# Kernel tuning notes

Measured on AMD Instinct MI355X. Metric: run time of the kernel, lower is better.

The kernel has to match this reference:

```python
import jax, jax.numpy as jnp
import numpy as np

N = 100000      # nodes
E = 1600000     # edges (avg degree 16)
F_IN = 48       # input features
H = 64          # hidden
C = 2           # classes


def _init(key, shape, fan_in):
    return jax.random.normal(key, shape, jnp.float32) * (1.0 / np.sqrt(fan_in))


def setup_inputs() -> dict:
    key = jax.random.key(0)
    ks = jax.random.split(key, 12)
    return {
        "x": jax.random.normal(ks[0], (N, F_IN), jnp.float32),
        "edge_index": jax.random.randint(ks[1], (2, E), 0, N, dtype=jnp.int64),
        "W1l": _init(ks[2], (F_IN, H), F_IN),
        "b1l": jnp.zeros((H,), jnp.float32),
        "W1r": _init(ks[3], (F_IN, H), F_IN),
        "W2l": _init(ks[4], (H, H), H),
        "b2l": jnp.zeros((H,), jnp.float32),
        "W2r": _init(ks[5], (H, H), H),
        "Wlin1": _init(ks[6], (H, H), H),
        "blin1": jnp.zeros((H,), jnp.float32),
        "Wlin2": _init(ks[7], (H, C), H),
        "blin2": jnp.zeros((C,), jnp.float32),
    }


def _sage_conv(x, src, dst, Wl, bl, Wr, num_nodes):
    # mean aggregation of source-node features onto destination nodes
    msg = x[src]                                              # [E, F] gather
    agg = jax.ops.segment_sum(msg, dst, num_segments=num_nodes)
    cnt = jax.ops.segment_sum(jnp.ones((dst.shape[0], 1), x.dtype), dst,
                              num_segments=num_nodes)
    mean = agg / jnp.maximum(cnt, 1.0)
    # PyG SAGEConv: lin_l(aggr) + lin_r(root); bias only on lin_l
    return mean @ Wl + bl + x @ Wr


def reference(x, edge_index, W1l, b1l, W1r, W2l, b2l, W2r,
              Wlin1, blin1, Wlin2, blin2):
    src, dst = edge_index[0], edge_index[1]
    n = x.shape[0]
    h = jax.nn.sigmoid(_sage_conv(x, src, dst, W1l, b1l, W1r, n))
    h = jax.nn.sigmoid(_sage_conv(h, src, dst, W2l, b2l, W2r, n))
    # dropout(p=0.5) is identity in eval mode (self.training=False)
    h = jax.nn.sigmoid(h @ Wlin1 + blin1)
    return jax.nn.softmax(h @ Wlin2 + blin2, axis=1)
```

## Files before the change

kernel.cpp:

```cpp
#include <hip/hip_runtime.h>
#include <math.h>


#define NF1 48
#define HH 64
#define BKT_SHIFT 8
#define BKT_SZ (1 << BKT_SHIFT)
#define BCAP 4800
#define EPB 16

typedef __attribute__((ext_vector_type(8))) short short8v;
typedef __attribute__((ext_vector_type(4))) float float4v;

__device__ __forceinline__ float sigmoidf_(float v) {
  return 1.0f / (1.0f + __expf(-v));
}
__device__ __forceinline__ float bflo(unsigned w) {
  union { unsigned u; float f; } c; c.u = w << 16; return c.f;
}
__device__ __forceinline__ float bfhi(unsigned w) {
  union { unsigned u; float f; } c; c.u = w & 0xffff0000u; return c.f;
}
__device__ __forceinline__ unsigned short f2bf(float f) {
  union { float f; unsigned u; } c; c.f = f;
  unsigned r = c.u + 0x7fffu + ((c.u >> 16) & 1u);
  return (unsigned short)(r >> 16);
}

template <int K>
__global__ __launch_bounds__(256, 4) void fused_bin_gemm(
    const int* __restrict__ ei, int* __restrict__ cursor,
    unsigned* __restrict__ bins, int E, int NB,
    const float* __restrict__ X, const float* __restrict__ Wl,
    const float* __restrict__ Wr, const float* __restrict__ bias,
    unsigned short* __restrict__ t_out, float* __restrict__ r_out,
    int n_nodes, int abk, int gemmb) {
  __shared__ __align__(16) char smem[3 * 64 * 72 * 2];

  if ((int)blockIdx.x < abk) {
    int* hist = (int*)smem;
    int* gbase = hist + 512;
    for (int i = threadIdx.x; i < NB; i += 256) hist[i] = 0;
    __syncthreads();
    int base_e = blockIdx.x * (256 * EPB) + threadIdx.x;
    unsigned pk[EPB];
    int bk[EPB], rk[EPB];
#pragma unroll
    for (int k = 0; k < EPB; k++) {
      int e = base_e + k * 256;
      bk[k] = -1;
      if (e < E) {
        int s = ei[e], d = ei[E + e];
        int b = d >> BKT_SHIFT;
        pk[k] = ((unsigned)(d & (BKT_SZ - 1)) << 23) | (unsigned)s;
        bk[k] = b;
        rk[k] = atomicAdd(&hist[b], 1);
      }
    }
    __syncthreads();
    for (int i = threadIdx.x; i < NB; i += 256) {
      int c = hist[i];
      gbase[i] = (c > 0) ? atomicAdd(&cursor[i], c) : 0;
    }
    __syncthreads();
#pragma unroll
    for (int k = 0; k < EPB; k++) {
      if (bk[k] >= 0) {
        int pos = gbase[bk[k]] + rk[k];
        bins[(size_t)bk[k] * BCAP + pos] = pk[k];
      }
    }
    return;
  }

  short(*sA)[72] = (short(*)[72])smem;
  short(*sWl)[72] = (short(*)[72])(smem + 9216);
  short(*sWr)[72] = (short(*)[72])(smem + 18432);
  int gbid = (int)blockIdx.x - abk;
  int lane = threadIdx.x & 63, wv = threadIdx.x >> 6;
  int l15 = lane & 15, kq = lane >> 4;

  for (int i = threadIdx.x; i < 64 * 64; i += 256) {
    int k = i >> 6, j = i & 63;
    short vl = 0, vr = 0;
    if (k < K) {
      vl = (short)f2bf(Wl[k * 64 + j]);
      vr = (short)f2bf(Wr[k * 64 + j]);
    }
    sWl[j][k] = vl;
    sWr[j][k] = vr;
  }
  if (K < 64) {
    constexpr int PADW = (64 - K) / 2;
    for (int i = threadIdx.x; i < 64 * PADW; i += 256) {
      int row = i / PADW, p = i % PADW;
      *(unsigned*)&sA[row][K + 2 * p] = 0u;
    }
  }
  float bcol[4];
#pragma unroll
  for (int c = 0; c < 4; c++) bcol[c] = bias[c * 16 + l15];

  for (int nbase = gbid * 64; nbase < n_nodes; nbase += gemmb * 64) {
    __syncthreads();
    for (int i = threadIdx.x; i < 64 * (K / 4); i += 256) {
      int row = i / (K / 4), c4 = i % (K / 4);
      int rr = nbase + row;
      if (rr >= n_nodes) rr = n_nodes - 1;
      float4 xv = ((const float4*)(X + (size_t)rr * K))[c4];
      unsigned lo = ((unsigned)f2bf(xv.y) << 16) | (unsigned)f2bf(xv.x);
      unsigned hi = ((unsigned)f2bf(xv.w) << 16) | (unsigned)f2bf(xv.z);
      uint2 pk2 = {lo, hi};
      *(uint2*)&sA[row][c4 * 4] = pk2;
    }
    __syncthreads();

    float4v acc_t[4], acc_r[4];
#pragma unroll
    for (int c = 0; c < 4; c++) {
      acc_t[c] = (float4v){0.0f, 0.0f, 0.0f, 0.0f};
      acc_r[c] = (float4v){bcol[c], bcol[c], bcol[c], bcol[c]};
    }
#pragma unroll
    for (int s = 0; s < 2; s++) {
      short8v af = *(const short8v*)&sA[wv * 16 + l15][s * 32 + kq * 8];
#pragma unroll
      for (int c = 0; c < 4; c++) {
        short8v bl = *(const short8v*)&sWl[c * 16 + l15][s * 32 + kq * 8];
        short8v br = *(const short8v*)&sWr[c * 16 + l15][s * 32 + kq * 8];
        acc_t[c] = __builtin_amdgcn_mfma_f32_16x16x32_bf16(af, bl, acc_t[c], 0, 0, 0);
        acc_r[c] = __builtin_amdgcn_mfma_f32_16x16x32_bf16(af, br, acc_r[c], 0, 0, 0);
      }
    }
#pragma unroll
    for (int c = 0; c < 4; c++) {
      int j = c * 16 + l15;
#pragma unroll
      for (int g = 0; g < 4; g++) {
        int node = nbase + wv * 16 + kq * 4 + g;
        if (node < n_nodes) {
          t_out[(size_t)node * HH + j] = f2bf(acc_t[c][g]);
          r_out[(size_t)node * HH + j] = acc_r[c][g];
        }
      }
    }
  }
}

__global__ __launch_bounds__(256) void build_csr2(
    const unsigned* __restrict__ bins, const int* __restrict__ cursor,
    int* __restrict__ rp, int* __restrict__ csr, int n_nodes, int E, int NB) {
  __shared__ int hist[BKT_SZ];
  __shared__ int aa[BKT_SZ], bb[BKT_SZ];
  __shared__ int cur[BKT_SZ];
  int b = blockIdx.x;
  int tid = threadIdx.x;
  int node0 = b << BKT_SHIFT;
  int cnt = cursor[b];
  const unsigned* bp = bins + (size_t)b * BCAP;

  int part = 0;
  for (int i = tid; i < b; i += 256) part += cursor[i];
  aa[tid] = part;
  __syncthreads();
  for (int off = 128; off > 0; off >>= 1) {
    if (tid < off) aa[tid] += aa[tid + off];
    __syncthreads();
  }
  int gb = aa[0];
  __syncthreads();

  hist[tid] = 0;
  __syncthreads();
  for (int i = tid; i < cnt; i += 256) {
    atomicAdd(&hist[bp[i] >> 23], 1);
  }
  __syncthreads();
  int v = hist[tid];
  aa[tid] = v;
  __syncthreads();
  int* s = aa;
  int* d = bb;
  for (int off = 1; off < BKT_SZ; off <<= 1) {
    int t = s[tid] + ((tid >= off) ? s[tid - off] : 0);
    d[tid] = t;
    __syncthreads();
    int* tmp = s; s = d; d = tmp;
  }
  int loc = s[tid] - v;
  int node = node0 + tid;
  if (node < n_nodes) rp[node] = gb + loc;
  if (b == NB - 1 && tid == 0) rp[n_nodes] = E;
  cur[tid] = gb + loc;
  __syncthreads();
  for (int i = tid; i < cnt; i += 256) {
    unsigned p = bp[i];
    int dl = (int)(p >> 23);
    int pos = atomicAdd(&cur[dl], 1);
    csr[pos] = (int)(p & 0x7FFFFFu);
  }
}

__device__ __forceinline__ void gather8(const uint4* __restrict__ tb,
                                        const int* __restrict__ csr,
                                        int rs, int re, float* __restrict__ a) {
  int j = rs;
  for (; j + 7 < re; j += 8) {
    uint4 u0 = tb[(size_t)csr[j + 0] * 8];
    uint4 u1 = tb[(size_t)csr[j + 1] * 8];
    uint4 u2 = tb[(size_t)csr[j + 2] * 8];
    uint4 u3 = tb[(size_t)csr[j + 3] * 8];
    uint4 u4 = tb[(size_t)csr[j + 4] * 8];
    uint4 u5 = tb[(size_t)csr[j + 5] * 8];
    uint4 u6 = tb[(size_t)csr[j + 6] * 8];
    uint4 u7 = tb[(size_t)csr[j + 7] * 8];
    a[0] += ((bflo(u0.x) + bflo(u1.x)) + (bflo(u2.x) + bflo(u3.x))) +
            ((bflo(u4.x) + bflo(u5.x)) + (bflo(u6.x) + bflo(u7.x)));
    a[1] += ((bfhi(u0.x) + bfhi(u1.x)) + (bfhi(u2.x) + bfhi(u3.x))) +
            ((bfhi(u4.x) + bfhi(u5.x)) + (bfhi(u6.x) + bfhi(u7.x)));
    a[2] += ((bflo(u0.y) + bflo(u1.y)) + (bflo(u2.y) + bflo(u3.y))) +
            ((bflo(u4.y) + bflo(u5.y)) + (bflo(u6.y) + bflo(u7.y)));
    a[3] += ((bfhi(u0.y) + bfhi(u1.y)) + (bfhi(u2.y) + bfhi(u3.y))) +
            ((bfhi(u4.y) + bfhi(u5.y)) + (bfhi(u6.y) + bfhi(u7.y)));
    a[4] += ((bflo(u0.z) + bflo(u1.z)) + (bflo(u2.z) + bflo(u3.z))) +
            ((bflo(u4.z) + bflo(u5.z)) + (bflo(u6.z) + bflo(u7.z)));
    a[5] += ((bfhi(u0.z) + bfhi(u1.z)) + (bfhi(u2.z) + bfhi(u3.z))) +
            ((bfhi(u4.z) + bfhi(u5.z)) + (bfhi(u6.z) + bfhi(u7.z)));
    a[6] += ((bflo(u0.w) + bflo(u1.w)) + (bflo(u2.w) + bflo(u3.w))) +
            ((bflo(u4.w) + bflo(u5.w)) + (bflo(u6.w) + bflo(u7.w)));
    a[7] += ((bfhi(u0.w) + bfhi(u1.w)) + (bfhi(u2.w) + bfhi(u3.w))) +
            ((bfhi(u4.w) + bfhi(u5.w)) + (bfhi(u6.w) + bfhi(u7.w)));
  }
  if (j + 3 < re) {
    uint4 u0 = tb[(size_t)csr[j + 0] * 8];
    uint4 u1 = tb[(size_t)csr[j + 1] * 8];
    uint4 u2 = tb[(size_t)csr[j + 2] * 8];
    uint4 u3 = tb[(size_t)csr[j + 3] * 8];
    a[0] += (bflo(u0.x) + bflo(u1.x)) + (bflo(u2.x) + bflo(u3.x));
    a[1] += (bfhi(u0.x) + bfhi(u1.x)) + (bfhi(u2.x) + bfhi(u3.x));
    a[2] += (bflo(u0.y) + bflo(u1.y)) + (bflo(u2.y) + bflo(u3.y));
    a[3] += (bfhi(u0.y) + bfhi(u1.y)) + (bfhi(u2.y) + bfhi(u3.y));
    a[4] += (bflo(u0.z) + bflo(u1.z)) + (bflo(u2.z) + bflo(u3.z));
    a[5] += (bfhi(u0.z) + bfhi(u1.z)) + (bfhi(u2.z) + bfhi(u3.z));
    a[6] += (bflo(u0.w) + bflo(u1.w)) + (bflo(u2.w) + bflo(u3.w));
    a[7] += (bfhi(u0.w) + bfhi(u1.w)) + (bfhi(u2.w) + bfhi(u3.w));
    j += 4;
  }
  for (; j < re; j++) {
    uint4 u = tb[(size_t)csr[j] * 8];
    a[0] += bflo(u.x);
    a[1] += bfhi(u.x);
    a[2] += bflo(u.y);
    a[3] += bfhi(u.y);
    a[4] += bflo(u.z);
    a[5] += bfhi(u.z);
    a[6] += bflo(u.w);
    a[7] += bfhi(u.w);
  }
}

__global__ __launch_bounds__(256, 4) void fused_agg_gemm(
    const unsigned short* __restrict__ t1, const float* __restrict__ r1,
    const int* __restrict__ rp, const int* __restrict__ csr,
    const float* __restrict__ W2l, const float* __restrict__ W2r,
    const float* __restrict__ b2l,
    unsigned short* __restrict__ t2, unsigned short* __restrict__ r2,
    int n_nodes, int gemmb) {
  __shared__ short sA[64][72];
  __shared__ short sWl[64][72];
  __shared__ short sWr[64][72];
  int lane = threadIdx.x & 63, wv = threadIdx.x >> 6;
  int l15 = lane & 15, kq = lane >> 4;
  int grp8 = threadIdx.x >> 3, q8 = threadIdx.x & 7;

  for (int i = threadIdx.x; i < 64 * 64; i += 256) {
    int k = i >> 6, j = i & 63;
    sWl[j][k] = (short)f2bf(W2l[k * 64 + j]);
    sWr[j][k] = (short)f2bf(W2r[k * 64 + j]);
  }
  float bcol[4];
#pragma unroll
  for (int c = 0; c < 4; c++) bcol[c] = b2l[c * 16 + l15];

  for (int nbase = blockIdx.x * 64; nbase < n_nodes; nbase += gemmb * 64) {
    __syncthreads();
#pragma unroll
    for (int p = 0; p < 2; p++) {
      int row = p * 32 + grp8;
      int node = nbase + row;
      int nn = node < n_nodes ? node : n_nodes - 1;
      int rs = rp[nn], re = rp[nn + 1];
      int deg = re - rs;
      float a[8] = {0, 0, 0, 0, 0, 0, 0, 0};
      gather8((const uint4*)t1 + q8, csr, rs, re, a);
      float inv = 1.0f / fmaxf((float)deg, 1.0f);
      float4 rv0 = ((const float4*)(r1 + (size_t)nn * HH))[2 * q8];
      float4 rv1 = ((const float4*)(r1 + (size_t)nn * HH))[2 * q8 + 1];
      float h0 = sigmoidf_(a[0] * inv + rv0.x);
      float h1v = sigmoidf_(a[1] * inv + rv0.y);
      float h2v = sigmoidf_(a[2] * inv + rv0.z);
      float h3v = sigmoidf_(a[3] * inv + rv0.w);
      float h4v = sigmoidf_(a[4] * inv + rv1.x);
      float h5v = sigmoidf_(a[5] * inv + rv1.y);
      float h6v = sigmoidf_(a[6] * inv + rv1.z);
      float h7v = sigmoidf_(a[7] * inv + rv1.w);
      uint4 pk;
      pk.x = ((unsigned)f2bf(h1v) << 16) | (unsigned)f2bf(h0);
      pk.y = ((unsigned)f2bf(h3v) << 16) | (unsigned)f2bf(h2v);
      pk.z = ((unsigned)f2bf(h5v) << 16) | (unsigned)f2bf(h4v);
      pk.w = ((unsigned)f2bf(h7v) << 16) | (unsigned)f2bf(h6v);
      *(uint4*)&sA[row][q8 * 8] = pk;
    }
    __syncthreads();

    float4v acc_t[4], acc_r[4];
#pragma unroll
    for (int c = 0; c < 4; c++) {
      acc_t[c] = (float4v){0.0f, 0.0f, 0.0f, 0.0f};
      acc_r[c] = (float4v){bcol[c], bcol[c], bcol[c], bcol[c]};
    }
#pragma unroll
    for (int s = 0; s < 2; s++) {
      short8v af = *(const short8v*)&sA[wv * 16 + l15][s * 32 + kq * 8];
#pragma unroll
      for (int c = 0; c < 4; c++) {
        short8v bl = *(const short8v*)&sWl[c * 16 + l15][s * 32 + kq * 8];
        short8v br = *(const short8v*)&sWr[c * 16 + l15][s * 32 + kq * 8];
        acc_t[c] = __builtin_amdgcn_mfma_f32_16x16x32_bf16(af, bl, acc_t[c], 0, 0, 0);
        acc_r[c] = __builtin_amdgcn_mfma_f32_16x16x32_bf16(af, br, acc_r[c], 0, 0, 0);
      }
    }
#pragma unroll
    for (int c = 0; c < 4; c++) {
      int j = c * 16 + l15;
#pragma unroll
      for (int g = 0; g < 4; g++) {
        int node = nbase + wv * 16 + kq * 4 + g;
        if (node < n_nodes) {
          t2[(size_t)node * HH + j] = f2bf(acc_t[c][g]);
          r2[(size_t)node * HH + j] = f2bf(acc_r[c][g]);
        }
      }
    }
  }
}

__global__ __launch_bounds__(256) void agg_sig_bf(
    const unsigned short* __restrict__ t, const unsigned short* __restrict__ r,
    const int* __restrict__ rp, const int* __restrict__ csr,
    float* __restrict__ h, int n_nodes) {
  int grp8 = threadIdx.x >> 3;
  int q8 = threadIdx.x & 7;
  int node = blockIdx.x * 32 + grp8;
  if (node >= n_nodes) return;
  int rs = rp[node], re = rp[node + 1];
  int deg = re - rs;

  float a[8] = {0, 0, 0, 0, 0, 0, 0, 0};
  gather8((const uint4*)t + q8, csr, rs, re, a);

  float inv = 1.0f / fmaxf((float)deg, 1.0f);
  uint4 ru = ((const uint4*)(r + (size_t)node * HH))[q8];
  float4 o0, o1;
  o0.x = sigmoidf_(a[0] * inv + bflo(ru.x));
  o0.y = sigmoidf_(a[1] * inv + bfhi(ru.x));
  o0.z = sigmoidf_(a[2] * inv + bflo(ru.y));
  o0.w = sigmoidf_(a[3] * inv + bfhi(ru.y));
  o1.x = sigmoidf_(a[4] * inv + bflo(ru.z));
  o1.y = sigmoidf_(a[5] * inv + bfhi(ru.z));
  o1.z = sigmoidf_(a[6] * inv + bflo(ru.w));
  o1.w = sigmoidf_(a[7] * inv + bfhi(ru.w));
  ((float4*)(h + (size_t)node * HH))[2 * q8 + 0] = o0;
  ((float4*)(h + (size_t)node * HH))[2 * q8 + 1] = o1;
}

__global__ __launch_bounds__(512, 4) void head_k(
    const float* __restrict__ h2,
    const float* __restrict__ Wlin1, const float* __restrict__ blin1,
    const float* __restrict__ Wlin2, const float* __restrict__ blin2,
    float* __restrict__ out, int n_nodes) {
  __shared__ float sx[64][HH];
  __shared__ float sh3[64][HH];
  __shared__ float sw2[HH * 2];
  int wv = threadIdx.x >> 6, lane = threadIdx.x & 63;

  float w1[HH];
#pragma unroll
  for (int k = 0; k < HH; k++) w1[k] = Wlin1[k * HH + lane];
  float bv = blin1[lane];
  if (threadIdx.x < HH * 2) sw2[threadIdx.x] = Wlin2[threadIdx.x];
  float sb20 = blin2[0], sb21 = blin2[1];

  for (int nbase = blockIdx.x * 64; nbase < n_nodes; nbase += gridDim.x * 64) {
    __syncthreads();
    for (int i = threadIdx.x; i < 64 * (HH / 4); i += 512) {
      int row = i >> 4, c4 = i & 15;
      int rr = nbase + row;
      if (rr >= n_nodes) rr = n_nodes - 1;
      ((float4*)sx[row])[c4] = ((const float4*)(h2 + (size_t)rr * HH))[c4];
    }
    __syncthreads();

    float acc[8];
#pragma unroll
    for (int m = 0; m < 8; m++) acc[m] = bv;
#pragma unroll
    for (int k = 0; k < HH; k += 4) {
#pragma unroll
      for (int m = 0; m < 8; m++) {
        float4 a = *(const float4*)&sx[wv * 8 + m][k];
        acc[m] += a.x * w1[k] + a.y * w1[k + 1] + a.z * w1[k + 2] + a.w * w1[k + 3];
      }
    }
#pragma unroll
    for (int m = 0; m < 8; m++) sh3[wv * 8 + m][lane] = sigmoidf_(acc[m]);
    __syncthreads();

    int node_l = threadIdx.x >> 3;
    int sub = threadIdx.x & 7;
    float l0 = 0.0f, l1 = 0.0f;
#pragma unroll
    for (int kk = 0; kk < 8; kk++) {
      int k = sub * 8 + kk;
      float v = sh3[node_l][k];
      l0 += v * sw2[k * 2 + 0];
      l1 += v * sw2[k * 2 + 1];
    }
    l0 += __shfl_xor(l0, 1); l1 += __shfl_xor(l1, 1);
    l0 += __shfl_xor(l0, 2); l1 += __shfl_xor(l1, 2);
    l0 += __shfl_xor(l0, 4); l1 += __shfl_xor(l1, 4);
    int node = nbase + node_l;
    if (sub == 0 && node < n_nodes) {
      l0 += sb20;
      l1 += sb21;
      float mx = fmaxf(l0, l1);
      float p0 = __expf(l0 - mx), p1 = __expf(l1 - mx);
      float s = 1.0f / (p0 + p1);
      float2 o2 = {p0 * s, p1 * s};
      ((float2*)out)[node] = o2;
    }
  }
}

extern "C" void kernel_launch(void* const* d_in, const int* in_sizes, int n_in,
                              void* d_out, int out_size, void* d_ws, size_t ws_size,
                              hipStream_t stream) {
  const float* x     = (const float*)d_in[0];
  const int*   ei    = (const int*)d_in[1];
  const float* W1l   = (const float*)d_in[2];
  const float* b1l   = (const float*)d_in[3];
  const float* W1r   = (const float*)d_in[4];
  const float* W2l   = (const float*)d_in[5];
  const float* b2l   = (const float*)d_in[6];
  const float* W2r   = (const float*)d_in[7];
  const float* Wlin1 = (const float*)d_in[8];
  const float* blin1 = (const float*)d_in[9];
  const float* Wlin2 = (const float*)d_in[10];
  const float* blin2 = (const float*)d_in[11];
  float* out = (float*)d_out;

  int n = in_sizes[0] / NF1;
  int E = in_sizes[1] / 2;
  int NB = (n + BKT_SZ - 1) >> BKT_SHIFT;

  int* cursor = (int*)d_ws;
  int* rp     = cursor + NB;
  int* csr    = rp + n + 1;
  size_t off = (size_t)(NB + n + 1 + E) * sizeof(int);
  off = (off + 255) & ~(size_t)255;
  size_t t1_off = off;
  unsigned short* t1 = (unsigned short*)((char*)d_ws + off);
  off += (size_t)n * HH * sizeof(unsigned short);
  off = (off + 255) & ~(size_t)255;
  float* r1 = (float*)((char*)d_ws + off);
  off += (size_t)n * HH * sizeof(float);
  off = (off + 255) & ~(size_t)255;
  unsigned short* t2 = (unsigned short*)((char*)d_ws + off);
  off += (size_t)n * HH * sizeof(unsigned short);
  off = (off + 255) & ~(size_t)255;
  unsigned short* r2 = (unsigned short*)((char*)d_ws + off);
  unsigned* bins = (unsigned*)t2;
  float* h2 = (float*)((char*)d_ws + t1_off);

  hipMemsetAsync(cursor, 0, (size_t)NB * sizeof(int), stream);

  int abk = (E + 256 * EPB - 1) / (256 * EPB);
  int chunks = (n + 63) / 64;
  int gemmb = chunks;
  int aggb = (n + 31) / 32;
  int headb = chunks;

  fused_bin_gemm<NF1><<<abk + gemmb, 256, 0, stream>>>(
      ei, cursor, bins, E, NB, x, W1l, W1r, b1l, t1, r1, n, abk, gemmb);

  build_csr2<<<NB, 256, 0, stream>>>(bins, cursor, rp, csr, n, E, NB);

  fused_agg_gemm<<<gemmb, 256, 0, stream>>>(t1, r1, rp, csr, W2l, W2r, b2l,
                                            t2, r2, n, gemmb);

  agg_sig_bf<<<aggb, 256, 0, stream>>>(t2, r2, rp, csr, h2, n);

  head_k<<<headb, 512, 0, stream>>>(h2, Wlin1, blin1, Wlin2, blin2, out, n);
}
```

Measured before the change: 168.8 us.

## Use persistent blocks with atomic work-stealing counters for GEMM and head kernels

Replaces the one-block-per-64-node-chunk grids of the two GEMM kernels and the head kernel with fixed-size persistent grids. Each block repeatedly claims a chunk through an atomic counter kept in the workspace and zeroed by the existing memset. The aim is to load the weight matrices into shared memory and registers once per block instead of once per chunk, and to balance work dynamically. The cost is an atomic plus two barriers per chunk, and the fixed grid sizes may not match the GPU's occupancy.

```diff
diff --git a/kernel.cpp b/kernel.cpp
--- a/kernel.cpp
+++ b/kernel.cpp
@@ -34,8 +34,9 @@
     const float* __restrict__ X, const float* __restrict__ Wl,
     const float* __restrict__ Wr, const float* __restrict__ bias,
     unsigned short* __restrict__ t_out, float* __restrict__ r_out,
-    int n_nodes, int abk, int gemmb) {
+    int n_nodes, int abk, int* __restrict__ ctr) {
   __shared__ __align__(16) char smem[3 * 64 * 72 * 2];
+  __shared__ int schunk;
 
   if ((int)blockIdx.x < abk) {
     int* hist = (int*)smem;
@@ -76,8 +77,8 @@
   short(*sA)[72] = (short(*)[72])smem;
   short(*sWl)[72] = (short(*)[72])(smem + 9216);
   short(*sWr)[72] = (short(*)[72])(smem + 18432);
-  int gbid = (int)blockIdx.x - abk;
-  int lane = threadIdx.x & 63, wv = threadIdx.x >> 6;
+  int lane = threadIdx.x & 63;
+  int wv = threadIdx.x >> 6;
   int l15 = lane & 15, kq = lane >> 4;
 
   for (int i = threadIdx.x; i < 64 * 64; i += 256) {
@@ -101,8 +102,13 @@
 #pragma unroll
   for (int c = 0; c < 4; c++) bcol[c] = bias[c * 16 + l15];
 
-  for (int nbase = gbid * 64; nbase < n_nodes; nbase += gemmb * 64) {
-    __syncthreads();
+  for (;;) {
+    __syncthreads();
+    if (threadIdx.x == 0) schunk = atomicAdd(ctr, 1);
+    __syncthreads();
+    int nbase = schunk * 64;
+    if (nbase >= n_nodes) break;
+
     for (int i = threadIdx.x; i < 64 * (K / 4); i += 256) {
       int row = i / (K / 4), c4 = i % (K / 4);
       int rr = nbase + row;
@@ -265,10 +271,11 @@
     const float* __restrict__ W2l, const float* __restrict__ W2r,
     const float* __restrict__ b2l,
     unsigned short* __restrict__ t2, unsigned short* __restrict__ r2,
-    int n_nodes, int gemmb) {
+    int n_nodes, int* __restrict__ ctr) {
   __shared__ short sA[64][72];
   __shared__ short sWl[64][72];
   __shared__ short sWr[64][72];
+  __shared__ int schunk;
   int lane = threadIdx.x & 63, wv = threadIdx.x >> 6;
   int l15 = lane & 15, kq = lane >> 4;
   int grp8 = threadIdx.x >> 3, q8 = threadIdx.x & 7;
@@ -282,8 +289,13 @@
 #pragma unroll
   for (int c = 0; c < 4; c++) bcol[c] = b2l[c * 16 + l15];
 
-  for (int nbase = blockIdx.x * 64; nbase < n_nodes; nbase += gemmb * 64) {
-    __syncthreads();
+  for (;;) {
+    __syncthreads();
+    if (threadIdx.x == 0) schunk = atomicAdd(ctr, 1);
+    __syncthreads();
+    int nbase = schunk * 64;
+    if (nbase >= n_nodes) break;
+
 #pragma unroll
     for (int p = 0; p < 2; p++) {
       int row = p * 32 + grp8;
@@ -378,10 +390,11 @@
     const float* __restrict__ h2,
     const float* __restrict__ Wlin1, const float* __restrict__ blin1,
     const float* __restrict__ Wlin2, const float* __restrict__ blin2,
-    float* __restrict__ out, int n_nodes) {
+    float* __restrict__ out, int n_nodes, int* __restrict__ ctr) {
   __shared__ float sx[64][HH];
   __shared__ float sh3[64][HH];
   __shared__ float sw2[HH * 2];
+  __shared__ int schunk;
   int wv = threadIdx.x >> 6, lane = threadIdx.x & 63;
 
   float w1[HH];
@@ -391,8 +404,13 @@
   if (threadIdx.x < HH * 2) sw2[threadIdx.x] = Wlin2[threadIdx.x];
   float sb20 = blin2[0], sb21 = blin2[1];
 
-  for (int nbase = blockIdx.x * 64; nbase < n_nodes; nbase += gridDim.x * 64) {
-    __syncthreads();
+  for (;;) {
+    __syncthreads();
+    if (threadIdx.x == 0) schunk = atomicAdd(ctr, 1);
+    __syncthreads();
+    int nbase = schunk * 64;
+    if (nbase >= n_nodes) break;
+
     for (int i = threadIdx.x; i < 64 * (HH / 4); i += 512) {
       int row = i >> 4, c4 = i & 15;
       int rr = nbase + row;
@@ -463,10 +481,11 @@
   int E = in_sizes[1] / 2;
   int NB = (n + BKT_SZ - 1) >> BKT_SHIFT;
 
-  int* cursor = (int*)d_ws;
+  int* ctrs   = (int*)d_ws;
+  int* cursor = ctrs + 4;
   int* rp     = cursor + NB;
   int* csr    = rp + n + 1;
-  size_t off = (size_t)(NB + n + 1 + E) * sizeof(int);
+  size_t off = (size_t)(4 + NB + n + 1 + E) * sizeof(int);
   off = (off + 255) & ~(size_t)255;
   size_t t1_off = off;
   unsigned short* t1 = (unsigned short*)((char*)d_ws + off);
@@ -482,23 +501,23 @@
   unsigned* bins = (unsigned*)t2;
   float* h2 = (float*)((char*)d_ws + t1_off);
 
-  hipMemsetAsync(cursor, 0, (size_t)NB * sizeof(int), stream);
+  hipMemsetAsync(d_ws, 0, (size_t)(4 + NB) * sizeof(int), stream);
 
   int abk = (E + 256 * EPB - 1) / (256 * EPB);
-  int chunks = (n + 63) / 64;
-  int gemmb = chunks;
   int aggb = (n + 31) / 32;
-  int headb = chunks;
-
-  fused_bin_gemm<NF1><<<abk + gemmb, 256, 0, stream>>>(
-      ei, cursor, bins, E, NB, x, W1l, W1r, b1l, t1, r1, n, abk, gemmb);
+  int gemm_res = 1280;
+  int head_res = 1024;
+
+  fused_bin_gemm<NF1><<<abk + gemm_res, 256, 0, stream>>>(
+      ei, cursor, bins, E, NB, x, W1l, W1r, b1l, t1, r1, n, abk, &ctrs[0]);
 
   build_csr2<<<NB, 256, 0, stream>>>(bins, cursor, rp, csr, n, E, NB);
 
-  fused_agg_gemm<<<gemmb, 256, 0, stream>>>(t1, r1, rp, csr, W2l, W2r, b2l,
-                                            t2, r2, n, gemmb);
+  fused_agg_gemm<<<gemm_res, 256, 0, stream>>>(t1, r1, rp, csr, W2l, W2r, b2l,
+                                               t2, r2, n, &ctrs[1]);
 
   agg_sig_bf<<<aggb, 256, 0, stream>>>(t2, r2, rp, csr, h2, n);
 
-  head_k<<<headb, 512, 0, stream>>>(h2, Wlin1, blin1, Wlin2, blin2, out, n);
-}
+  head_k<<<head_res, 512, 0, stream>>>(h2, Wlin1, blin1, Wlin2, blin2, out, n,
+                                       &ctrs[2]);
+}
```

Measured after the change: 207.0 us. 22.6% more time.
